# Kernel tuning notes

Hardware: AMD Instinct MI355X
Metric: run time of the kernel (lower is better)

## Reference

```python
import jax, jax.numpy as jnp
import numpy as np

POOL = 7
IMG = 1024.0
NUM_CLASSES = 2
R = 1000


def crop_and_resize(feat, boxes, pool):
    # feat: [C,H,W]; boxes: [N,4] normalized (y1,x1,y2,x2); returns [N,C,pool,pool]
    C, H, W = feat.shape
    y1, x1, y2, x2 = boxes[:, 0], boxes[:, 1], boxes[:, 2], boxes[:, 3]
    t = jnp.arange(pool, dtype=feat.dtype) / (pool - 1)
    ys = (y1[:, None] + (y2 - y1)[:, None] * t[None, :]) * (H - 1)  # [N,P]
    xs = (x1[:, None] + (x2 - x1)[:, None] * t[None, :]) * (W - 1)  # [N,P]
    vy = (ys >= 0) & (ys <= H - 1)
    vx = (xs >= 0) & (xs <= W - 1)
    yf = jnp.floor(ys)
    xf = jnp.floor(xs)
    wy = (ys - yf)[None, :, :, None]  # [1,N,P,1]
    wx = (xs - xf)[None, :, None, :]  # [1,N,1,P]
    y0 = jnp.clip(yf, 0, H - 1).astype(jnp.int32)
    y1i = jnp.clip(yf + 1, 0, H - 1).astype(jnp.int32)
    x0 = jnp.clip(xf, 0, W - 1).astype(jnp.int32)
    x1i = jnp.clip(xf + 1, 0, W - 1).astype(jnp.int32)

    def g(yi, xi):  # gather -> [C,N,P,P]
        return feat[:, yi[:, :, None], xi[:, None, :]]

    val = (g(y0, x0) * (1 - wy) * (1 - wx)
           + g(y0, x1i) * (1 - wy) * wx
           + g(y1i, x0) * wy * (1 - wx)
           + g(y1i, x1i) * wy * wx)
    mask = (vy[:, :, None] & vx[:, None, :])[None]  # extrapolation value 0
    return jnp.where(mask, val, 0.0).transpose(1, 0, 2, 3)


def roi_align(feats, rois_flat):
    # rois_flat: [N,4] in pixel coords (x1,y1,x2,y2)
    x1, y1, x2, y2 = rois_flat[:, 0], rois_flat[:, 1], rois_flat[:, 2], rois_flat[:, 3]
    lvl = jnp.log2(jnp.sqrt((y2 - y1) * (x2 - x1)) / 224.0)
    lvl = jnp.clip(jnp.round(lvl) + 4, 2, 5)
    boxes = rois_flat[:, jnp.array([1, 0, 3, 2])] / IMG  # (y1,x1,y2,x2) normalized
    crops = jnp.stack([crop_and_resize(f[0], boxes, POOL) for f in feats])  # [4,N,C,P,P]
    sel = (lvl[None, :] == jnp.arange(2, 6, dtype=lvl.dtype)[:, None])       # [4,N]
    return jnp.sum(jnp.where(sel[:, :, None, None, None], crops, 0.0), axis=0)  # [N,C,P,P]


def setup_inputs() -> dict:
    key = jax.random.key(0)
    ks = jax.random.split(key, 24)
    feat2 = jax.random.normal(ks[0], (1, 256, 256, 256), jnp.float32)
    feat3 = jax.random.normal(ks[1], (1, 256, 128, 128), jnp.float32)
    feat4 = jax.random.normal(ks[2], (1, 256, 64, 64), jnp.float32)
    feat5 = jax.random.normal(ks[3], (1, 256, 32, 32), jnp.float32)
    x1 = jax.random.uniform(ks[4], (1, R), minval=0.0, maxval=900.0)
    y1 = jax.random.uniform(ks[5], (1, R), minval=0.0, maxval=900.0)
    w = jax.random.uniform(ks[6], (1, R), minval=16.0, maxval=400.0)
    h = jax.random.uniform(ks[7], (1, R), minval=16.0, maxval=400.0)
    rois = jnp.stack([x1, y1, jnp.minimum(x1 + w, 1023.0), jnp.minimum(y1 + h, 1023.0)], axis=-1)
    s = 0.02
    params = dict(
        conv_w=s * jax.random.normal(ks[8], (1024, 256, POOL, POOL), jnp.float32),
        conv_b=jnp.zeros((1024,), jnp.float32),
        bn_gamma=jnp.ones((1024,), jnp.float32),
        bn_beta=jnp.zeros((1024,), jnp.float32),
        bn_mean=jnp.zeros((1024,), jnp.float32),
        bn_var=jnp.ones((1024,), jnp.float32),
        fc1_w=s * jax.random.normal(ks[9], (1024, 1024), jnp.float32),
        fc1_b=jnp.zeros((1024,), jnp.float32),
        fc2_w=s * jax.random.normal(ks[10], (1024, 1024), jnp.float32),
        fc2_b=jnp.zeros((1024,), jnp.float32),
        cls_w=s * jax.random.normal(ks[11], (NUM_CLASSES, 1024), jnp.float32),
        cls_b=jnp.zeros((NUM_CLASSES,), jnp.float32),
        bbox_w=s * jax.random.normal(ks[12], (NUM_CLASSES * 4, 1024), jnp.float32),
        bbox_b=jnp.zeros((NUM_CLASSES * 4,), jnp.float32),
    )
    return dict(feat2=feat2, feat3=feat3, feat4=feat4, feat5=feat5, rois=rois, **params)


def reference(feat2, feat3, feat4, feat5, rois, conv_w, conv_b, bn_gamma, bn_beta,
              bn_mean, bn_var, fc1_w, fc1_b, fc2_w, fc2_b, cls_w, cls_b, bbox_w, bbox_b):
    roi_number = rois.shape[1]
    pooled = roi_align([feat2, feat3, feat4, feat5], rois.reshape(-1, 4))  # [N,256,7,7]
    # conv1 (7x7 valid on 7x7 input -> 1x1 spatial) + BN (inference stats, eps=1e-3)
    y = jnp.einsum('nchw,ochw->no', pooled, conv_w) + conv_b
    y = (y - bn_mean) / jnp.sqrt(bn_var + 1e-3) * bn_gamma + bn_beta
    h = jax.nn.relu(y @ fc1_w.T + fc1_b)
    h = jax.nn.relu(h @ fc2_w.T + fc2_b)
    logits = h @ cls_w.T + cls_b
    probs = jax.nn.softmax(logits, axis=-1)
    bbox = h @ bbox_w.T + bbox_b
    return (logits.reshape(1, roi_number, NUM_CLASSES),
            probs.reshape(1, roi_number, NUM_CLASSES),
            bbox.reshape(1, roi_number, NUM_CLASSES, 4))
```

## Files before the change

### kernel.cpp

```cpp
#include <hip/hip_runtime.h>
#include <cstdint>
#include <cstddef>

typedef __attribute__((ext_vector_type(8))) short bf16x8;
typedef __attribute__((ext_vector_type(4))) float f32x4;

#define POOLK 12544

#define TOFF2 0
#define TOFF3 16777216
#define TOFF4 20971520
#define TOFF5 22020096

__device__ __forceinline__ void gld16(const void* g, void* l) {
    __builtin_amdgcn_global_load_lds(
        (const __attribute__((address_space(1))) void*)g,
        (__attribute__((address_space(3))) void*)l, 16, 0, 0);
}
__device__ __forceinline__ unsigned short f32_to_bf16(float f) {
    union { float f; unsigned u; } x; x.f = f;
    return (unsigned short)((x.u + 0x7FFFu + ((x.u >> 16) & 1u)) >> 16);
}
__device__ __forceinline__ float bf16_to_f32(unsigned short s) {
    return __uint_as_float(((unsigned)s) << 16);
}

__global__ __launch_bounds__(256) void feat_tr_kernel(
    const float* __restrict__ f2, const float* __restrict__ f3,
    const float* __restrict__ f4, const float* __restrict__ f5,
    unsigned short* __restrict__ T)
{
    __shared__ __align__(16) unsigned short sh[128 * 256];
    int b = blockIdx.x;
    const float* src; unsigned short* dst; int P;
    if (b < 512)      { src = f2; dst = T + TOFF2; P = 65536; }
    else if (b < 640) { src = f3; dst = T + TOFF3; P = 16384; b -= 512; }
    else if (b < 672) { src = f4; dst = T + TOFF4; P = 4096;  b -= 640; }
    else              { src = f5; dst = T + TOFF5; P = 1024;  b -= 672; }
    const int p0 = b * 128;
    const int t = threadIdx.x;
    const int lane5 = t & 31;
    const int x4 = lane5 * 4;
    const int fx = (lane5 & 7) << 3;

#pragma unroll
    for (int it = 0; it < 8; ++it) {
        float4 v[4];
        int cs[4];
#pragma unroll
        for (int u = 0; u < 4; ++u) {
            cs[u] = it * 32 + u * 8 + (t >> 5);
            v[u] = *(const float4*)(src + (size_t)cs[u] * P + p0 + x4);
        }
#pragma unroll
        for (int u = 0; u < 4; ++u) {
            const int cp = cs[u] ^ fx;
            float vv[4] = {v[u].x, v[u].y, v[u].z, v[u].w};
#pragma unroll
            for (int i = 0; i < 4; ++i)
                sh[(x4 + i) * 256 + cp] = f32_to_bf16(vv[i]);
        }
    }
    __syncthreads();

    const int c0 = lane5 * 8;
#pragma unroll
    for (int oz = 0; oz < 16; ++oz) {
        const int pp = oz * 8 + (t >> 5);
        const int cr = c0 ^ (((pp >> 2) & 7) << 3);
        const bf16x8 vv = *(const bf16x8*)&sh[pp * 256 + cr];
        *(bf16x8*)(dst + (size_t)(p0 + pp) * 256 + c0) = vv;
    }
}

__global__ __launch_bounds__(256) void gather_prep_kernel(
    const unsigned short* __restrict__ T, const float* __restrict__ rois,
    unsigned short* __restrict__ pooled, int nroi,
    const float* __restrict__ conv_w, unsigned short* __restrict__ convw_bf,
    const float* __restrict__ fc1_w, unsigned short* __restrict__ fc1w_bf,
    const float* __restrict__ fc2_w, unsigned short* __restrict__ fc2w_bf)
{
    const int t = threadIdx.x;
    const int grp = blockIdx.x / 7, rem = blockIdx.x % 7;

    if (rem >= 4) {
        if (rem < 6) {
            const int o = grp * 2 + (rem - 4);
            __shared__ __align__(16) unsigned short shw[POOLK];
            const float* srow = conv_w + (size_t)o * POOLK;
            for (int k4 = t; k4 < 3136; k4 += 256) {
                const float4 v = *(const float4*)(srow + k4 * 4);
                ushort4 o4;
                o4.x = f32_to_bf16(v.x); o4.y = f32_to_bf16(v.y);
                o4.z = f32_to_bf16(v.z); o4.w = f32_to_bf16(v.w);
                *(ushort4*)(&shw[k4 * 4]) = o4;
            }
            __syncthreads();
            unsigned short* drow = convw_bf + (size_t)o * POOLK;
            for (int e = t; e < 1568; e += 256) {
                const int p = e * 8;
                const int ij = p >> 8, c0 = p & 255;
                bf16x8 o8;
#pragma unroll
                for (int c = 0; c < 8; ++c) o8[c] = (short)shw[(c0 + c) * 49 + ij];
                *(bf16x8*)(drow + p) = o8;
            }
        } else {
            const int bb = grp;
            const float* src = (bb < 256) ? fc1_w : fc2_w;
            unsigned short* dst = (bb < 256) ? fc1w_bf : fc2w_bf;
            const int base = (bb & 255) * 4096 + t * 16;
#pragma unroll
            for (int u = 0; u < 4; ++u) {
                const float4 v = *(const float4*)(src + base + u * 4);
                ushort4 o4;
                o4.x = f32_to_bf16(v.x); o4.y = f32_to_bf16(v.y);
                o4.z = f32_to_bf16(v.z); o4.w = f32_to_bf16(v.w);
                *(ushort4*)(dst + base + u * 4) = o4;
            }
        }
        return;
    }

    const int gb = grp * 4 + rem;
    const int n = gb >> 1;
    const int half = gb & 1;
    unsigned short* orow = pooled + (size_t)n * POOLK;
    if (n >= nroi) {
        const bf16x8 z = {};
        const int base = half * 6272;
        for (int k = base + t * 8; k < base + 6272; k += 2048) *(bf16x8*)(orow + k) = z;
        return;
    }
    __shared__ int sy0[7], sy1[7], sx0[7], sx1[7];
    __shared__ float swy[7], swx[7], svy[7], svx[7];

    const float rx1 = rois[n*4+0], ry1 = rois[n*4+1];
    const float rx2 = rois[n*4+2], ry2 = rois[n*4+3];
    int lvl = (int)rintf(log2f(sqrtf((ry2-ry1)*(rx2-rx1)) * (1.0f/224.0f))) + 4;
    lvl = lvl < 2 ? 2 : (lvl > 5 ? 5 : lvl);
    const int W = 256 >> (lvl - 2);
    const float Hm1 = (float)(W - 1);
    const unsigned short* Tl = T + (lvl == 2 ? TOFF2 : (lvl == 3 ? TOFF3 : (lvl == 4 ? TOFF4 : TOFF5)));

    if (t < 7) {
        const float tt = (float)t / 6.0f;
        const float by1 = ry1*(1.0f/1024.0f), by2 = ry2*(1.0f/1024.0f);
        const float bx1 = rx1*(1.0f/1024.0f), bx2 = rx2*(1.0f/1024.0f);
        const float ys = (by1 + (by2 - by1) * tt) * Hm1;
        const float xs = (bx1 + (bx2 - bx1) * tt) * Hm1;
        const float yf = floorf(ys), xf = floorf(xs);
        swy[t] = ys - yf;  swx[t] = xs - xf;
        sy0[t] = (int)fminf(fmaxf(yf,        0.0f), Hm1);
        sy1[t] = (int)fminf(fmaxf(yf + 1.0f, 0.0f), Hm1);
        sx0[t] = (int)fminf(fmaxf(xf,        0.0f), Hm1);
        sx1[t] = (int)fminf(fmaxf(xf + 1.0f, 0.0f), Hm1);
        svy[t] = (ys >= 0.0f && ys <= Hm1) ? 1.0f : 0.0f;
        svx[t] = (xs >= 0.0f && xs <= Hm1) ? 1.0f : 0.0f;
    }
    __syncthreads();

    const int g    = t >> 5;
    const int c0   = (t & 31) * 8;
    const int pbeg = half * 25;
    const int pend = pbeg + 25 - half;
#pragma unroll
    for (int it = 0; it < 4; ++it) {
        const int pos = pbeg + it * 8 + g;
        if (pos >= pend) break;
        const int i = pos / 7, j = pos % 7;
        const int y0 = sy0[i], y1 = sy1[i], x0 = sx0[j], x1 = sx1[j];
        const float wy = swy[i], wx = swx[j];
        const float scale = svy[i] * svx[j];
        const bf16x8 v00 = *(const bf16x8*)(Tl + ((size_t)(y0*W + x0))*256 + c0);
        const bf16x8 v01 = *(const bf16x8*)(Tl + ((size_t)(y0*W + x1))*256 + c0);
        const bf16x8 v10 = *(const bf16x8*)(Tl + ((size_t)(y1*W + x0))*256 + c0);
        const bf16x8 v11 = *(const bf16x8*)(Tl + ((size_t)(y1*W + x1))*256 + c0);
        bf16x8 o;
#pragma unroll
        for (int jj = 0; jj < 8; ++jj) {
            const float f00 = bf16_to_f32((unsigned short)v00[jj]);
            const float f01 = bf16_to_f32((unsigned short)v01[jj]);
            const float f10 = bf16_to_f32((unsigned short)v10[jj]);
            const float f11 = bf16_to_f32((unsigned short)v11[jj]);
            const float top = f00 + (f01 - f00) * wx;
            const float bot = f10 + (f11 - f10) * wx;
            o[jj] = (short)f32_to_bf16((top + (bot - top) * wy) * scale);
        }
        *(bf16x8*)(orow + pos * 256 + c0) = o;
    }
}

__global__ __launch_bounds__(256) void roi_direct_kernel(
    const float* __restrict__ feat2, const float* __restrict__ feat3,
    const float* __restrict__ feat4, const float* __restrict__ feat5,
    const float* __restrict__ rois, unsigned short* __restrict__ pooled, int nroi)
{
    const int n = blockIdx.x;
    const int tid = threadIdx.x;
    unsigned short* orow = pooled + (size_t)n * POOLK;
    if (n >= nroi) {
        const bf16x8 z = {};
        for (int k = tid * 8; k < POOLK; k += 2048) *(bf16x8*)(orow + k) = z;
        return;
    }
    __shared__ int sy0[7], sy1[7], sx0[7], sx1[7];
    __shared__ float swy[7], swx[7], svy[7], svx[7];
    const float rx1 = rois[n*4+0], ry1 = rois[n*4+1];
    const float rx2 = rois[n*4+2], ry2 = rois[n*4+3];
    int lvl = (int)rintf(log2f(sqrtf((ry2-ry1)*(rx2-rx1)) * (1.0f/224.0f))) + 4;
    lvl = lvl < 2 ? 2 : (lvl > 5 ? 5 : lvl);
    const int H = 256 >> (lvl - 2);
    const float Hm1 = (float)(H - 1);
    const float* feat = lvl==2 ? feat2 : (lvl==3 ? feat3 : (lvl==4 ? feat4 : feat5));
    if (tid < 7) {
        const float t = (float)tid / 6.0f;
        const float by1 = ry1*(1.0f/1024.0f), by2 = ry2*(1.0f/1024.0f);
        const float bx1 = rx1*(1.0f/1024.0f), bx2 = rx2*(1.0f/1024.0f);
        const float ys = (by1 + (by2-by1)*t) * Hm1;
        const float xs = (bx1 + (bx2-bx1)*t) * Hm1;
        const float yf = floorf(ys), xf = floorf(xs);
        swy[tid] = ys - yf;  swx[tid] = xs - xf;
        sy0[tid] = (int)fminf(fmaxf(yf,      0.0f), Hm1);
        sy1[tid] = (int)fminf(fmaxf(yf+1.0f, 0.0f), Hm1);
        sx0[tid] = (int)fminf(fmaxf(xf,      0.0f), Hm1);
        sx1[tid] = (int)fminf(fmaxf(xf+1.0f, 0.0f), Hm1);
        svy[tid] = (ys >= 0.0f && ys <= Hm1) ? 1.0f : 0.0f;
        svx[tid] = (xs >= 0.0f && xs <= Hm1) ? 1.0f : 0.0f;
    }
    __syncthreads();
    const int HW = H * H;
    for (int e = tid; e < POOLK; e += 256) {
        const int c = e / 49, ij = e % 49, i = ij / 7, j = ij % 7;
        const float* p = feat + c * HW;
        const int y0 = sy0[i], y1 = sy1[i], x0 = sx0[j], x1 = sx1[j];
        const float wy = swy[i], wx = swx[j];
        const float v00 = p[y0*H + x0], v01 = p[y0*H + x1];
        const float v10 = p[y1*H + x0], v11 = p[y1*H + x1];
        float v = v00*(1.0f-wy)*(1.0f-wx) + v01*(1.0f-wy)*wx
                + v10*wy*(1.0f-wx)        + v11*wy*wx;
        v *= svy[i] * svx[j];
        orow[ij*256 + c] = f32_to_bf16(v);
    }
}

__global__ __launch_bounds__(256) void wprep_kernel(
    const float* __restrict__ conv_w, unsigned short* __restrict__ convw_bf,
    const float* __restrict__ fc1_w, unsigned short* __restrict__ fc1w_bf,
    const float* __restrict__ fc2_w, unsigned short* __restrict__ fc2w_bf)
{
    const int t = threadIdx.x;
    int b = blockIdx.x;
    if (b < 1024) {
        __shared__ __align__(16) unsigned short shw[POOLK];
        const float* srow = conv_w + (size_t)b * POOLK;
        for (int k4 = t; k4 < 3136; k4 += 256) {
            const float4 v = *(const float4*)(srow + k4 * 4);
            ushort4 o4;
            o4.x = f32_to_bf16(v.x); o4.y = f32_to_bf16(v.y);
            o4.z = f32_to_bf16(v.z); o4.w = f32_to_bf16(v.w);
            *(ushort4*)(&shw[k4 * 4]) = o4;
        }
        __syncthreads();
        unsigned short* drow = convw_bf + (size_t)b * POOLK;
        for (int e = t; e < 1568; e += 256) {
            const int p = e * 8;
            const int ij = p >> 8, c0 = p & 255;
            bf16x8 o8;
#pragma unroll
            for (int c = 0; c < 8; ++c) o8[c] = (short)shw[(c0 + c) * 49 + ij];
            *(bf16x8*)(drow + p) = o8;
        }
        return;
    }
    b -= 1024;
    const float* src = (b < 256) ? fc1_w : fc2_w;
    unsigned short* dst = (b < 256) ? fc1w_bf : fc2w_bf;
    const int base = (b & 255) * 4096 + t * 16;
#pragma unroll
    for (int u = 0; u < 4; ++u) {
        const float4 v = *(const float4*)(src + base + u * 4);
        ushort4 o4;
        o4.x = f32_to_bf16(v.x); o4.y = f32_to_bf16(v.y);
        o4.z = f32_to_bf16(v.z); o4.w = f32_to_bf16(v.w);
        *(ushort4*)(dst + base + u * 4) = o4;
    }
}

__global__ __launch_bounds__(256, 2) void gemm_bt(
    const unsigned short* __restrict__ A, const unsigned short* __restrict__ B,
    unsigned short* __restrict__ Cpart, int K, int Kper, int nz)
{
    __shared__ __align__(16) unsigned short At[2][128*64];
    __shared__ __align__(16) unsigned short Bt[2][128*64];
    const int tid  = threadIdx.x;
    const int lane = tid & 63;
    const int bid  = blockIdx.x;
    const int z  = bid % nz;
    const int iq = bid / nz;
    const int bx = iq & 7, by = iq >> 3;
    const int wm = (tid >> 6) >> 1, wn = (tid >> 6) & 1;
    const size_t k0 = (size_t)z * Kper;

    const int r1 = tid >> 3;
    const int q  = tid & 7;
    const int csw = (q ^ (r1 & 7)) * 8;
    const unsigned short* Ag = A + ((size_t)(by * 128 + r1)) * K + k0 + csw;
    const unsigned short* Bg = B + ((size_t)(bx * 128 + r1)) * K + k0 + csw;
    const int nit = (Kper + 63) >> 6;

#pragma unroll
    for (int p = 0; p < 4; ++p) {
        gld16(Ag + (size_t)(32 * p) * K, &At[0][p * 2048 + tid * 8]);
        gld16(Bg + (size_t)(32 * p) * K, &Bt[0][p * 2048 + tid * 8]);
    }

    f32x4 acc[4][4] = {};
    const int fr = lane & 15;
    const int fq = lane >> 4;
    const int sA = fr & 7;

    int buf = 0;
    for (int it = 0; it < nit; ++it) {
        const int k = it << 6;
        if (it + 1 < nit) {
            const size_t ko = (size_t)(k + 64);
#pragma unroll
            for (int p = 0; p < 4; ++p) {
                gld16(Ag + (size_t)(32 * p) * K + ko, &At[buf ^ 1][p * 2048 + tid * 8]);
                gld16(Bg + (size_t)(32 * p) * K + ko, &Bt[buf ^ 1][p * 2048 + tid * 8]);
            }
            asm volatile("s_waitcnt vmcnt(8)" ::: "memory");
        } else {
            asm volatile("s_waitcnt vmcnt(0)" ::: "memory");
        }
        __builtin_amdgcn_sched_barrier(0);
        __builtin_amdgcn_s_barrier();
        __builtin_amdgcn_sched_barrier(0);

        bf16x8 a[4][2], b[4][2];
#pragma unroll
        for (int mi = 0; mi < 4; ++mi) {
            const int row = wm * 64 + mi * 16 + fr;
#pragma unroll
            for (int kk = 0; kk < 2; ++kk)
                a[mi][kk] = *(const bf16x8*)&At[buf][row * 64 + ((kk * 4 + fq) ^ sA) * 8];
        }
#pragma unroll
        for (int ni = 0; ni < 4; ++ni) {
            const int row = wn * 64 + ni * 16 + fr;
#pragma unroll
            for (int kk = 0; kk < 2; ++kk)
                b[ni][kk] = *(const bf16x8*)&Bt[buf][row * 64 + ((kk * 4 + fq) ^ sA) * 8];
        }
        __builtin_amdgcn_s_setprio(1);
#pragma unroll
        for (int mi = 0; mi < 4; ++mi)
#pragma unroll
            for (int ni = 0; ni < 4; ++ni)
                acc[mi][ni] = __builtin_amdgcn_mfma_f32_16x16x32_bf16(
                    a[mi][0], b[ni][0], acc[mi][ni], 0, 0, 0);
        if (k + 32 < Kper) {
#pragma unroll
            for (int mi = 0; mi < 4; ++mi)
#pragma unroll
                for (int ni = 0; ni < 4; ++ni)
                    acc[mi][ni] = __builtin_amdgcn_mfma_f32_16x16x32_bf16(
                        a[mi][1], b[ni][1], acc[mi][ni], 0, 0, 0);
        }
        __builtin_amdgcn_s_setprio(0);
        __builtin_amdgcn_sched_barrier(0);
        __builtin_amdgcn_s_barrier();
        __builtin_amdgcn_sched_barrier(0);
        buf ^= 1;
    }

    unsigned short* Cp = Cpart + (size_t)z * (1024 * 1024);
    const int row0 = by * 128 + wm * 64;
    const int col0 = bx * 128 + wn * 64;
#pragma unroll
    for (int mi = 0; mi < 4; ++mi)
#pragma unroll
        for (int ni = 0; ni < 4; ++ni)
#pragma unroll
            for (int r = 0; r < 4; ++r)
                Cp[(size_t)(row0 + mi*16 + fq*4 + r) * 1024 + col0 + ni*16 + fr]
                    = f32_to_bf16(acc[mi][ni][r]);
}

__global__ void reduce_bn_kernel(const unsigned short* __restrict__ part,
    const float* __restrict__ bias, const float* __restrict__ gamma,
    const float* __restrict__ beta, const float* __restrict__ mean,
    const float* __restrict__ var, unsigned short* __restrict__ out, int nz)
{
    const int i4 = (blockIdx.x * 256 + threadIdx.x) * 4;
    const int n = i4 & 1023;
    float4 v = make_float4(0.f, 0.f, 0.f, 0.f);
    for (int zz = 0; zz < nz; ++zz) {
        const ushort4 p = *(const ushort4*)(part + (size_t)zz * 1048576 + i4);
        v.x += bf16_to_f32(p.x); v.y += bf16_to_f32(p.y);
        v.z += bf16_to_f32(p.z); v.w += bf16_to_f32(p.w);
    }
    const float4 bi = *(const float4*)(bias + n);
    const float4 ga = *(const float4*)(gamma + n);
    const float4 be = *(const float4*)(beta + n);
    const float4 me = *(const float4*)(mean + n);
    const float4 va = *(const float4*)(var + n);
    ushort4 o;
    o.x = f32_to_bf16((v.x + bi.x - me.x) * __frsqrt_rn(va.x + 0.001f) * ga.x + be.x);
    o.y = f32_to_bf16((v.y + bi.y - me.y) * __frsqrt_rn(va.y + 0.001f) * ga.y + be.y);
    o.z = f32_to_bf16((v.z + bi.z - me.z) * __frsqrt_rn(va.z + 0.001f) * ga.z + be.z);
    o.w = f32_to_bf16((v.w + bi.w - me.w) * __frsqrt_rn(va.w + 0.001f) * ga.w + be.w);
    *(ushort4*)(out + i4) = o;
}

__global__ __launch_bounds__(256) void gemm64_fused(
    const unsigned short* __restrict__ A, const unsigned short* __restrict__ B,
    const float* __restrict__ bias, unsigned short* __restrict__ out, int relu)
{
    __shared__ __align__(16) unsigned short At[2][64*64];
    __shared__ __align__(16) unsigned short Bt[2][64*64];
    const int tid = threadIdx.x, lane = tid & 63;
    const int w = tid >> 6, wm = w >> 1, wn = w & 1;
    const int r1 = tid >> 3;
    const int q  = tid & 7;
    const int csw = (q ^ (r1 & 7)) * 8;
    const unsigned short* Ag = A + (size_t)(blockIdx.y*64 + r1) * 1024 + csw;
    const unsigned short* Bg = B + (size_t)(blockIdx.x*64 + r1) * 1024 + csw;
    const int fr = lane & 15, fq = lane >> 4;
    const int sA = fr & 7;

#pragma unroll
    for (int p = 0; p < 2; ++p) {
        gld16(Ag + (size_t)(32 * p) * 1024, &At[0][p * 2048 + tid * 8]);
        gld16(Bg + (size_t)(32 * p) * 1024, &Bt[0][p * 2048 + tid * 8]);
    }

    f32x4 acc[2][2] = {};
    int buf = 0;
    for (int it = 0; it < 16; ++it) {
        if (it + 1 < 16) {
            const int ko = (it + 1) * 64;
#pragma unroll
            for (int p = 0; p < 2; ++p) {
                gld16(Ag + (size_t)(32 * p) * 1024 + ko, &At[buf ^ 1][p * 2048 + tid * 8]);
                gld16(Bg + (size_t)(32 * p) * 1024 + ko, &Bt[buf ^ 1][p * 2048 + tid * 8]);
            }
            asm volatile("s_waitcnt vmcnt(4)" ::: "memory");
        } else {
            asm volatile("s_waitcnt vmcnt(0)" ::: "memory");
        }
        __builtin_amdgcn_sched_barrier(0);
        __builtin_amdgcn_s_barrier();
        __builtin_amdgcn_sched_barrier(0);

        bf16x8 a[2][2], b[2][2];
#pragma unroll
        for (int mi = 0; mi < 2; ++mi) {
            const int row = wm * 32 + mi * 16 + fr;
#pragma unroll
            for (int kk = 0; kk < 2; ++kk)
                a[mi][kk] = *(const bf16x8*)&At[buf][row * 64 + ((kk * 4 + fq) ^ sA) * 8];
        }
#pragma unroll
        for (int ni = 0; ni < 2; ++ni) {
            const int row = wn * 32 + ni * 16 + fr;
#pragma unroll
            for (int kk = 0; kk < 2; ++kk)
                b[ni][kk] = *(const bf16x8*)&Bt[buf][row * 64 + ((kk * 4 + fq) ^ sA) * 8];
        }
        __builtin_amdgcn_s_setprio(1);
#pragma unroll
        for (int kk = 0; kk < 2; ++kk)
#pragma unroll
            for (int mi = 0; mi < 2; ++mi)
#pragma unroll
                for (int ni = 0; ni < 2; ++ni)
                    acc[mi][ni] = __builtin_amdgcn_mfma_f32_16x16x32_bf16(
                        a[mi][kk], b[ni][kk], acc[mi][ni], 0, 0, 0);
        __builtin_amdgcn_s_setprio(0);
        __builtin_amdgcn_sched_barrier(0);
        __builtin_amdgcn_s_barrier();
        __builtin_amdgcn_sched_barrier(0);
        buf ^= 1;
    }
    const int row0 = blockIdx.y*64 + wm*32;
    const int col0 = blockIdx.x*64 + wn*32;
#pragma unroll
    for (int mi = 0; mi < 2; ++mi)
#pragma unroll
        for (int ni = 0; ni < 2; ++ni)
#pragma unroll
            for (int r = 0; r < 4; ++r) {
                const int row = row0 + mi*16 + fq*4 + r;
                const int col = col0 + ni*16 + fr;
                float v = acc[mi][ni][r] + bias[col];
                if (relu) v = fmaxf(v, 0.0f);
                out[(size_t)row * 1024 + col] = f32_to_bf16(v);
            }
}

__global__ __launch_bounds__(256) void head_kernel(
    const unsigned short* __restrict__ h2,
    const float* __restrict__ cls_w, const float* __restrict__ cls_b,
    const float* __restrict__ bbox_w, const float* __restrict__ bbox_b,
    float* __restrict__ out)
{
    const int roi = blockIdx.x * 4 + (threadIdx.x >> 6);
    const int lane = threadIdx.x & 63;
    const unsigned short* hrow = h2 + (size_t)roi * 1024;
    float hv[16];
#pragma unroll
    for (int j = 0; j < 16; ++j)
        hv[j] = bf16_to_f32(hrow[lane*16 + j]);
    float r[10];
#pragma unroll
    for (int o = 0; o < 10; ++o) {
        const float* w = (o < 2) ? (cls_w + o*1024) : (bbox_w + (size_t)(o-2)*1024);
        float s = 0.f;
#pragma unroll
        for (int j = 0; j < 16; ++j) s += hv[j] * w[lane*16 + j];
#pragma unroll
        for (int off = 32; off > 0; off >>= 1) s += __shfl_xor(s, off);
        r[o] = s;
    }
    if (lane == 0) {
        const float l0 = r[0] + cls_b[0], l1 = r[1] + cls_b[1];
        out[roi*2+0] = l0; out[roi*2+1] = l1;
        const float m = fmaxf(l0, l1);
        const float e0 = expf(l0 - m), e1 = expf(l1 - m);
        const float inv = 1.0f / (e0 + e1);
        out[2000 + roi*2 + 0] = e0 * inv;
        out[2000 + roi*2 + 1] = e1 * inv;
#pragma unroll
        for (int qq = 0; qq < 8; ++qq) out[4000 + roi*8 + qq] = r[2+qq] + bbox_b[qq];
    }
}

extern "C" void kernel_launch(void* const* d_in, const int* in_sizes, int n_in,
                              void* d_out, int out_size, void* d_ws, size_t ws_size,
                              hipStream_t stream)
{
    const float* feat2   = (const float*)d_in[0];
    const float* feat3   = (const float*)d_in[1];
    const float* feat4   = (const float*)d_in[2];
    const float* feat5   = (const float*)d_in[3];
    const float* rois    = (const float*)d_in[4];
    const float* conv_w  = (const float*)d_in[5];
    const float* conv_b  = (const float*)d_in[6];
    const float* bn_gamma= (const float*)d_in[7];
    const float* bn_beta = (const float*)d_in[8];
    const float* bn_mean = (const float*)d_in[9];
    const float* bn_var  = (const float*)d_in[10];
    const float* fc1_w   = (const float*)d_in[11];
    const float* fc1_b   = (const float*)d_in[12];
    const float* fc2_w   = (const float*)d_in[13];
    const float* fc2_b   = (const float*)d_in[14];
    const float* cls_w   = (const float*)d_in[15];
    const float* cls_b   = (const float*)d_in[16];
    const float* bbox_w  = (const float*)d_in[17];
    const float* bbox_b  = (const float*)d_in[18];
    float* out = (float*)d_out;
    const int nroi = in_sizes[4] / 4;

    const size_t fixedBytes = (size_t)25690112 + 25690112 + 5 * (size_t)2097152;
    const size_t needA = fixedBytes + (size_t)44564480;
    const int tier = (ws_size >= needA) ? 1 : 2;
    const size_t regionA = tier == 1 ? (size_t)44564480 : (size_t)16777216;
    const int nzc  = tier == 1 ? 8 : 4;
    const int Kper = tier == 1 ? 1568 : 3136;

    char* ws = (char*)d_ws;
    size_t off = 0;
    auto alloc = [&](size_t bytes) {
        void* p = ws + off; off += (bytes + 255) & ~(size_t)255; return p;
    };
    char* rA = (char*)alloc(regionA);
    unsigned short* T    = (unsigned short*)rA;
    unsigned short* part = (unsigned short*)rA;
    unsigned short* pooled   = (unsigned short*)alloc((size_t)1024 * POOLK * 2);
    unsigned short* convw_bf = (unsigned short*)alloc((size_t)1024 * POOLK * 2);
    unsigned short* fc1w_bf  = (unsigned short*)alloc((size_t)1048576 * 2);
    unsigned short* fc2w_bf  = (unsigned short*)alloc((size_t)1048576 * 2);
    unsigned short* ybf      = (unsigned short*)alloc((size_t)1048576 * 2);
    unsigned short* h1bf     = (unsigned short*)alloc((size_t)1048576 * 2);
    unsigned short* h2bf     = (unsigned short*)alloc((size_t)1048576 * 2);

    if (tier == 1) {
        hipLaunchKernelGGL(feat_tr_kernel, dim3(680), dim3(256), 0, stream,
                           feat2, feat3, feat4, feat5, T);
        hipLaunchKernelGGL(gather_prep_kernel, dim3(3584), dim3(256), 0, stream,
                           T, rois, pooled, nroi,
                           conv_w, convw_bf, fc1_w, fc1w_bf, fc2_w, fc2w_bf);
    } else {
        hipLaunchKernelGGL(wprep_kernel, dim3(1536), dim3(256), 0, stream,
                           conv_w, convw_bf, fc1_w, fc1w_bf, fc2_w, fc2w_bf);
        hipLaunchKernelGGL(roi_direct_kernel, dim3(1024), dim3(256), 0, stream,
                           feat2, feat3, feat4, feat5, rois, pooled, nroi);
    }

    hipLaunchKernelGGL(gemm_bt, dim3(64 * nzc), dim3(256), 0, stream,
                       pooled, convw_bf, part, POOLK, Kper, nzc);
    hipLaunchKernelGGL(reduce_bn_kernel, dim3(1024), dim3(256), 0, stream,
                       part, conv_b, bn_gamma, bn_beta, bn_mean, bn_var, ybf, nzc);

    hipLaunchKernelGGL(gemm64_fused, dim3(16, 16), dim3(256), 0, stream,
                       ybf, fc1w_bf, fc1_b, h1bf, 1);
    hipLaunchKernelGGL(gemm64_fused, dim3(16, 16), dim3(256), 0, stream,
                       h1bf, fc2w_bf, fc2_b, h2bf, 1);

    hipLaunchKernelGGL(head_kernel, dim3(250), dim3(256), 0, stream,
                       h2bf, cls_w, cls_b, bbox_w, bbox_b, out);
}
```

Baseline: 125.3 us.

## Pad conv K dimension and switch conv GEMM to 16-way split-K with BK=32

The pooled activations and conv weights are now stored with row stride 12800 instead of 12544, and every producer writes zeros into the padding. This lets K split evenly into 16 chunks of 800 (8 chunks of 1600 on the fallback tier). The conv GEMM drops its double-buffered BK=64 pipeline for a single-buffered BK=32 loop with plain syncthreads. Launch bounds rise to 4 waves per SIMD so latency is hidden by occupancy rather than by prefetch. The trade-off is twice as many split-K partials for the BN reduce kernel to read, some extra zero MACs, and exposed load latency on every iteration.

```diff
diff --git a/kernel.cpp b/kernel.cpp
--- a/kernel.cpp
+++ b/kernel.cpp
@@ -6,6 +6,7 @@
 typedef __attribute__((ext_vector_type(4))) float f32x4;
 
 #define POOLK 12544
+#define KPAD  12800
 
 #define TOFF2 0
 #define TOFF3 16777216
@@ -82,6 +83,7 @@
 {
     const int t = threadIdx.x;
     const int grp = blockIdx.x / 7, rem = blockIdx.x % 7;
+    const bf16x8 z8 = {};
 
     if (rem >= 4) {
         if (rem < 6) {
@@ -96,7 +98,7 @@
                 *(ushort4*)(&shw[k4 * 4]) = o4;
             }
             __syncthreads();
-            unsigned short* drow = convw_bf + (size_t)o * POOLK;
+            unsigned short* drow = convw_bf + (size_t)o * KPAD;
             for (int e = t; e < 1568; e += 256) {
                 const int p = e * 8;
                 const int ij = p >> 8, c0 = p & 255;
@@ -105,6 +107,7 @@
                 for (int c = 0; c < 8; ++c) o8[c] = (short)shw[(c0 + c) * 49 + ij];
                 *(bf16x8*)(drow + p) = o8;
             }
+            if (t < 32) *(bf16x8*)(drow + POOLK + t * 8) = z8;
         } else {
             const int bb = grp;
             const float* src = (bb < 256) ? fc1_w : fc2_w;
@@ -125,11 +128,10 @@
     const int gb = grp * 4 + rem;
     const int n = gb >> 1;
     const int half = gb & 1;
-    unsigned short* orow = pooled + (size_t)n * POOLK;
+    unsigned short* orow = pooled + (size_t)n * KPAD;
     if (n >= nroi) {
-        const bf16x8 z = {};
-        const int base = half * 6272;
-        for (int k = base + t * 8; k < base + 6272; k += 2048) *(bf16x8*)(orow + k) = z;
+        const int kend = half ? KPAD : 6272;
+        for (int k = half * 6272 + t * 8; k < kend; k += 2048) *(bf16x8*)(orow + k) = z8;
         return;
     }
     __shared__ int sy0[7], sy1[7], sx0[7], sx1[7];
@@ -160,6 +162,8 @@
     }
     __syncthreads();
 
+    if (half && t < 32) *(bf16x8*)(orow + POOLK + t * 8) = z8;
+
     const int g    = t >> 5;
     const int c0   = (t & 31) * 8;
     const int pbeg = half * 25;
@@ -198,12 +202,13 @@
 {
     const int n = blockIdx.x;
     const int tid = threadIdx.x;
-    unsigned short* orow = pooled + (size_t)n * POOLK;
+    unsigned short* orow = pooled + (size_t)n * KPAD;
+    const bf16x8 z8 = {};
     if (n >= nroi) {
-        const bf16x8 z = {};
-        for (int k = tid * 8; k < POOLK; k += 2048) *(bf16x8*)(orow + k) = z;
+        for (int k = tid * 8; k < KPAD; k += 2048) *(bf16x8*)(orow + k) = z8;
         return;
     }
+    if (tid < 32) *(bf16x8*)(orow + POOLK + tid * 8) = z8;
     __shared__ int sy0[7], sy1[7], sx0[7], sx1[7];
     __shared__ float swy[7], swx[7], svy[7], svx[7];
     const float rx1 = rois[n*4+0], ry1 = rois[n*4+1];
@@ -262,7 +267,7 @@
             *(ushort4*)(&shw[k4 * 4]) = o4;
         }
         __syncthreads();
-        unsigned short* drow = convw_bf + (size_t)b * POOLK;
+        unsigned short* drow = convw_bf + (size_t)b * KPAD;
         for (int e = t; e < 1568; e += 256) {
             const int p = e * 8;
             const int ij = p >> 8, c0 = p & 255;
@@ -271,6 +276,8 @@
             for (int c = 0; c < 8; ++c) o8[c] = (short)shw[(c0 + c) * 49 + ij];
             *(bf16x8*)(drow + p) = o8;
         }
+        const bf16x8 z8 = {};
+        if (t < 32) *(bf16x8*)(drow + POOLK + t * 8) = z8;
         return;
     }
     b -= 1024;
@@ -287,92 +294,60 @@
     }
 }
 
-__global__ __launch_bounds__(256, 2) void gemm_bt(
+__global__ __launch_bounds__(256, 4) void gemm_bt(
     const unsigned short* __restrict__ A, const unsigned short* __restrict__ B,
     unsigned short* __restrict__ Cpart, int K, int Kper, int nz)
 {
-    __shared__ __align__(16) unsigned short At[2][128*64];
-    __shared__ __align__(16) unsigned short Bt[2][128*64];
+    __shared__ __align__(16) unsigned short At[128 * 32];
+    __shared__ __align__(16) unsigned short Bt[128 * 32];
     const int tid  = threadIdx.x;
     const int lane = tid & 63;
     const int bid  = blockIdx.x;
-    const int z  = bid % nz;
-    const int iq = bid / nz;
+    int z, iq;
+    if (nz == 16) { z = (bid & 7) * 2 + ((bid >> 3) & 1); iq = bid >> 4; }
+    else          { z = bid % nz;                          iq = bid / nz; }
     const int bx = iq & 7, by = iq >> 3;
     const int wm = (tid >> 6) >> 1, wn = (tid >> 6) & 1;
     const size_t k0 = (size_t)z * Kper;
 
-    const int r1 = tid >> 3;
-    const int q  = tid & 7;
-    const int csw = (q ^ (r1 & 7)) * 8;
+    const int r1 = tid >> 2;
+    const int csw = (((tid & 3) ^ ((tid >> 3) & 3))) * 8;
     const unsigned short* Ag = A + ((size_t)(by * 128 + r1)) * K + k0 + csw;
     const unsigned short* Bg = B + ((size_t)(bx * 128 + r1)) * K + k0 + csw;
-    const int nit = (Kper + 63) >> 6;
-
-#pragma unroll
-    for (int p = 0; p < 4; ++p) {
-        gld16(Ag + (size_t)(32 * p) * K, &At[0][p * 2048 + tid * 8]);
-        gld16(Bg + (size_t)(32 * p) * K, &Bt[0][p * 2048 + tid * 8]);
-    }
+    const int nit = Kper >> 5;
 
     f32x4 acc[4][4] = {};
     const int fr = lane & 15;
     const int fq = lane >> 4;
-    const int sA = fr & 7;
-
-    int buf = 0;
+    const int sx = (fr >> 1) & 3;
+
     for (int it = 0; it < nit; ++it) {
-        const int k = it << 6;
-        if (it + 1 < nit) {
-            const size_t ko = (size_t)(k + 64);
-#pragma unroll
-            for (int p = 0; p < 4; ++p) {
-                gld16(Ag + (size_t)(32 * p) * K + ko, &At[buf ^ 1][p * 2048 + tid * 8]);
-                gld16(Bg + (size_t)(32 * p) * K + ko, &Bt[buf ^ 1][p * 2048 + tid * 8]);
-            }
-            asm volatile("s_waitcnt vmcnt(8)" ::: "memory");
-        } else {
-            asm volatile("s_waitcnt vmcnt(0)" ::: "memory");
-        }
-        __builtin_amdgcn_sched_barrier(0);
-        __builtin_amdgcn_s_barrier();
-        __builtin_amdgcn_sched_barrier(0);
-
-        bf16x8 a[4][2], b[4][2];
+        const size_t ko = (size_t)it * 32;
+        gld16(Ag + ko,                  &At[tid * 8]);
+        gld16(Ag + (size_t)64 * K + ko, &At[(tid + 256) * 8]);
+        gld16(Bg + ko,                  &Bt[tid * 8]);
+        gld16(Bg + (size_t)64 * K + ko, &Bt[(tid + 256) * 8]);
+        asm volatile("s_waitcnt vmcnt(0)" ::: "memory");
+        __syncthreads();
+
+        bf16x8 a[4], b[4];
 #pragma unroll
         for (int mi = 0; mi < 4; ++mi) {
-            const int row = wm * 64 + mi * 16 + fr;
-#pragma unroll
-            for (int kk = 0; kk < 2; ++kk)
-                a[mi][kk] = *(const bf16x8*)&At[buf][row * 64 + ((kk * 4 + fq) ^ sA) * 8];
+            const int m = wm * 64 + mi * 16 + fr;
+            a[mi] = *(const bf16x8*)&At[m * 32 + ((fq ^ sx) << 3)];
         }
 #pragma unroll
         for (int ni = 0; ni < 4; ++ni) {
-            const int row = wn * 64 + ni * 16 + fr;
-#pragma unroll
-            for (int kk = 0; kk < 2; ++kk)
-                b[ni][kk] = *(const bf16x8*)&Bt[buf][row * 64 + ((kk * 4 + fq) ^ sA) * 8];
-        }
-        __builtin_amdgcn_s_setprio(1);
+            const int m = wn * 64 + ni * 16 + fr;
+            b[ni] = *(const bf16x8*)&Bt[m * 32 + ((fq ^ sx) << 3)];
+        }
 #pragma unroll
         for (int mi = 0; mi < 4; ++mi)
 #pragma unroll
             for (int ni = 0; ni < 4; ++ni)
                 acc[mi][ni] = __builtin_amdgcn_mfma_f32_16x16x32_bf16(
-                    a[mi][0], b[ni][0], acc[mi][ni], 0, 0, 0);
-        if (k + 32 < Kper) {
-#pragma unroll
-            for (int mi = 0; mi < 4; ++mi)
-#pragma unroll
-                for (int ni = 0; ni < 4; ++ni)
-                    acc[mi][ni] = __builtin_amdgcn_mfma_f32_16x16x32_bf16(
-                        a[mi][1], b[ni][1], acc[mi][ni], 0, 0, 0);
-        }
-        __builtin_amdgcn_s_setprio(0);
-        __builtin_amdgcn_sched_barrier(0);
-        __builtin_amdgcn_s_barrier();
-        __builtin_amdgcn_sched_barrier(0);
-        buf ^= 1;
+                    a[mi], b[ni], acc[mi][ni], 0, 0, 0);
+        __syncthreads();
     }
 
     unsigned short* Cp = Cpart + (size_t)z * (1024 * 1024);
@@ -563,12 +538,13 @@
     float* out = (float*)d_out;
     const int nroi = in_sizes[4] / 4;
 
-    const size_t fixedBytes = (size_t)25690112 + 25690112 + 5 * (size_t)2097152;
+    const size_t poolBytes = (size_t)1024 * KPAD * 2;
+    const size_t fixedBytes = 2 * poolBytes + 5 * (size_t)2097152;
     const size_t needA = fixedBytes + (size_t)44564480;
     const int tier = (ws_size >= needA) ? 1 : 2;
     const size_t regionA = tier == 1 ? (size_t)44564480 : (size_t)16777216;
-    const int nzc  = tier == 1 ? 8 : 4;
-    const int Kper = tier == 1 ? 1568 : 3136;
+    const int nzc  = tier == 1 ? 16 : 8;
+    const int Kper = tier == 1 ? 800 : 1600;
 
     char* ws = (char*)d_ws;
     size_t off = 0;
@@ -578,8 +554,8 @@
     char* rA = (char*)alloc(regionA);
     unsigned short* T    = (unsigned short*)rA;
     unsigned short* part = (unsigned short*)rA;
-    unsigned short* pooled   = (unsigned short*)alloc((size_t)1024 * POOLK * 2);
-    unsigned short* convw_bf = (unsigned short*)alloc((size_t)1024 * POOLK * 2);
+    unsigned short* pooled   = (unsigned short*)alloc(poolBytes);
+    unsigned short* convw_bf = (unsigned short*)alloc(poolBytes);
     unsigned short* fc1w_bf  = (unsigned short*)alloc((size_t)1048576 * 2);
     unsigned short* fc2w_bf  = (unsigned short*)alloc((size_t)1048576 * 2);
     unsigned short* ybf      = (unsigned short*)alloc((size_t)1048576 * 2);
@@ -600,7 +576,7 @@
     }
 
     hipLaunchKernelGGL(gemm_bt, dim3(64 * nzc), dim3(256), 0, stream,
-                       pooled, convw_bf, part, POOLK, Kper, nzc);
+                       pooled, convw_bf, part, KPAD, Kper, nzc);
     hipLaunchKernelGGL(reduce_bn_kernel, dim3(1024), dim3(256), 0, stream,
                        part, conv_b, bn_gamma, bn_beta, bn_mean, bn_var, ybf, nzc);
 
```

After: 125.8 us. No clear change (+0.4%).
